# Kernel optimization log

Hardware: AMD Instinct MI355X
Metric: run time of the kernel (lower is better)

Reference implementation:

```python
import jax, jax.numpy as jnp
import numpy as np


def _cell(x, h, c, Wih, Whh, bih, bhh):
    # PyTorch LSTMCell: gates = x@Wih^T + bih + h@Whh^T + bhh, gate order i,f,g,o
    g = x @ Wih.T + bih + h @ Whh.T + bhh
    i, f, gg, o = jnp.split(g, 4, axis=-1)
    c_new = jax.nn.sigmoid(f) * c + jax.nn.sigmoid(i) * jnp.tanh(gg)
    h_new = jax.nn.sigmoid(o) * jnp.tanh(c_new)
    return h_new, c_new


def _forward(input, covariates, W_ih0, W_hh0, b_ih0, b_hh0,
             W_ih_r, W_hh_r, b_ih_r, b_hh_r, Wl, bl, future):
    B, T, _ = input.shape
    H = W_hh0.shape[1]
    Lm1 = W_ih_r.shape[0]  # number of stacked cells after layer 0

    # conditioning inputs: concat series with covariates -> [T, B, input_dim]
    xs = jnp.swapaxes(jnp.concatenate([input, covariates[:, :T, :]], axis=2), 0, 1)

    h0 = jnp.zeros((B, H), input.dtype)
    c0 = jnp.zeros((B, H), input.dtype)
    hr = jnp.zeros((Lm1, B, H), input.dtype)
    cr = jnp.zeros((Lm1, B, H), input.dtype)

    def run(state, x_t):
        h0, c0, hr, cr = state
        h0, c0 = _cell(x_t, h0, c0, W_ih0, W_hh0, b_ih0, b_hh0)
        prev = h0
        hs, cs = [], []
        for n in range(Lm1):  # static small loop over layers
            hn, cn = _cell(prev, hr[n], cr[n], W_ih_r[n], W_hh_r[n], b_ih_r[n], b_hh_r[n])
            hs.append(hn); cs.append(cn)
            prev = hn
        out = prev @ Wl.T + bl  # [B, output_dim]
        return (h0, c0, jnp.stack(hs), jnp.stack(cs)), out

    state, outs_cond = jax.lax.scan(run, (h0, c0, hr, cr), xs)  # outs_cond: [T,B,out]

    if future > 0:
        cov_f = jnp.swapaxes(covariates[:, T:T + future, :], 0, 1)  # [F,B,cov]

        def fut(carry, cov_t):
            state, out = carry
            x_t = jnp.concatenate([out, cov_t], axis=1)
            state, out = run(state, x_t)
            return (state, out), out

        _, outs_fut = jax.lax.scan(fut, (state, outs_cond[-1]), cov_f)
        outs = jnp.concatenate([outs_cond, outs_fut], axis=0)
    else:
        outs = outs_cond
    return jnp.swapaxes(outs, 0, 1)  # [B, T+future, output_dim]


def setup_inputs() -> dict:
    key = jax.random.key(0)
    ks = jax.random.split(key, 12)
    B, T, F = 512, 256, 64
    H, IN, COV, OUT, L = 1024, 8, 7, 1, 4
    s = 0.05
    return {
        "input": jax.random.normal(ks[0], (B, T, OUT), dtype=jnp.float32),
        "covariates": jax.random.normal(ks[1], (B, T + F, COV), dtype=jnp.float32),
        "W_ih0": jax.random.normal(ks[2], (4 * H, IN), dtype=jnp.float32) * s,
        "W_hh0": jax.random.normal(ks[3], (4 * H, H), dtype=jnp.float32) * s,
        "b_ih0": jax.random.normal(ks[4], (4 * H,), dtype=jnp.float32) * s,
        "b_hh0": jax.random.normal(ks[5], (4 * H,), dtype=jnp.float32) * s,
        "W_ih_r": jax.random.normal(ks[6], (L - 1, 4 * H, H), dtype=jnp.float32) * s,
        "W_hh_r": jax.random.normal(ks[7], (L - 1, 4 * H, H), dtype=jnp.float32) * s,
        "b_ih_r": jax.random.normal(ks[8], (L - 1, 4 * H), dtype=jnp.float32) * s,
        "b_hh_r": jax.random.normal(ks[9], (L - 1, 4 * H), dtype=jnp.float32) * s,
        "Wl": jax.random.normal(ks[10], (OUT, H), dtype=jnp.float32) * s,
        "bl": jax.random.normal(ks[11], (OUT,), dtype=jnp.float32) * s,
        "future": F,
    }


def reference(input, covariates, W_ih0, W_hh0, b_ih0, b_hh0,
              W_ih_r, W_hh_r, b_ih_r, b_hh_r, Wl, bl, future):
    return _forward(input, covariates, W_ih0, W_hh0, b_ih0, b_hh0,
                    W_ih_r, W_hh_r, b_ih_r, b_hh_r, Wl, bl, future)
```

## Files before the change

### kernel.cpp

```cpp
#include <hip/hip_runtime.h>

typedef _Float16 f16;
typedef __attribute__((ext_vector_type(8))) _Float16 half8;
typedef __attribute__((ext_vector_type(4))) float f32x4;
typedef __attribute__((ext_vector_type(4))) unsigned int uint4v;

#define B_   512
#define T_   256
#define TT_  320
#define KB0  33
#define KBR  64
#define NSLOT 12

#define AUX_COHERENT 17

struct PP {
  const f16* Wt[4];
  f16* xh[4][2];
  float* cst;
  const float* bias;
  const float* input;
  const float* cov;
  const float* Wl;
  const float* blp;
  float* out;
  unsigned* cnt;
};

__device__ __forceinline__ void gload16(const void* g, void* l) {
  __builtin_amdgcn_global_load_lds((const __attribute__((address_space(1))) void*)g,
                                   (__attribute__((address_space(3))) void*)l,
                                   16, 0, 0);
}
__device__ __forceinline__ void gload16c(const void* g, void* l) {
  __builtin_amdgcn_global_load_lds((const __attribute__((address_space(1))) void*)g,
                                   (__attribute__((address_space(3))) void*)l,
                                   16, 0, AUX_COHERENT);
}

__device__ __forceinline__ float sigf(float x) {
  return __builtin_amdgcn_rcpf(1.f + __builtin_amdgcn_exp2f(-1.44269504f * x));
}
__device__ __forceinline__ float tanhf_(float x) {
  return 2.f * __builtin_amdgcn_rcpf(1.f + __builtin_amdgcn_exp2f(-2.88539008f * x)) - 1.f;
}

__device__ __forceinline__ int haddr(int k, int m) {
  return (k >> 5) * 16384 + (m >> 4) * 512 + ((m & 15) + ((k & 31) >> 3) * 16) * 8 + (k & 7);
}

#define WAITBAR(vm) asm volatile("s_waitcnt vmcnt(" #vm ") lgkmcnt(0)\n\ts_barrier" ::: "memory")

__global__ __launch_bounds__(512, 2) void lstm_cond(PP P)
{
  __shared__ f16 lds[6][12288];
  const int tid = threadIdx.x;
  const int ln = tid & 63, w = tid >> 6;
  const int mg = w >> 2, ng = w & 3;
  const int cid = blockIdx.x >> 6, bb = blockIdx.x & 63;
  const int mb2 = bb >> 4, nb2 = bb & 15;
  const int m0 = mb2 * 128;
  const int l = cid;

  const f16* __restrict__ Wt = P.Wt[l];
  const int KB   = (l == 0) ? KB0 : KBR;
  const int koff = (l == 0) ? 32 : 1024;
  const float* __restrict__ bias4 = P.bias + l * 4096;
  float* __restrict__ cst = P.cst + (size_t)l * 524288;
  const int col = (nb2 * 4 + ng) * 16 + (ln & 15);
  const float bi  = bias4[col];
  const float bff = bias4[1024 + col];
  const float bgg = bias4[2048 + col];
  const float bo  = bias4[3072 + col];
  const float wl  = (l == 3) ? P.Wl[col] : 0.f;

  for (int s = 0; s <= 258; ++s) {
    if (s > 0) {
      if (tid == 0) {
        while (__hip_atomic_load(&P.cnt[s - 1], __ATOMIC_RELAXED,
                                 __HIP_MEMORY_SCOPE_AGENT) < 256u)
          __builtin_amdgcn_s_sleep(8);
      }
      __syncthreads();
    }

    const int t = s - l;
    if (t >= 0 && t < T_) {
      const int p = t & 1, q = p ^ 1;
      const f16* __restrict__ src = P.xh[l][p];
      f16* __restrict__ selfd     = P.xh[l][q];
      f16* __restrict__ nextd     = (l < 3) ? P.xh[l + 1][p] : nullptr;

      if (l == 0 && nb2 == 0 && tid < 128)
        __hip_atomic_store(&P.out[(size_t)(m0 + tid) * TT_ + t], P.blp[0],
                           __ATOMIC_RELAXED, __HIP_MEMORY_SCOPE_AGENT);

      auto stage_slab = [&](int slot, int kb) {
        if (l == 0 && kb == 0) {
          int mf = tid >> 6, r = ln & 15, kgrp = ln >> 4;
          int brow = m0 + mf * 16 + r;
          half8 v;
          #pragma unroll
          for (int j = 0; j < 8; ++j) v[j] = (f16)0.f;
          if (kgrp == 0) {
            v[0] = (f16)P.input[brow * T_ + t];
            const float* cp = P.cov + ((size_t)brow * TT_ + t) * 7;
            #pragma unroll
            for (int j = 1; j < 8; ++j) v[j] = (f16)cp[j - 1];
          }
          *(half8*)&lds[slot][tid * 8] = v;
        } else {
          gload16c(src + (size_t)kb * 16384 + mb2 * 4096 + tid * 8, &lds[slot][tid * 8]);
        }
        {
          const int e0 = tid, e1 = tid + 512;
          gload16(Wt + ((size_t)((nb2 * 4 + (e0 >> 8)) * KB + kb)) * 2048 + (e0 & 255) * 8,
                  &lds[slot][4096 + e0 * 8]);
          gload16(Wt + ((size_t)((nb2 * 4 + (e1 >> 8)) * KB + kb)) * 2048 + (e1 & 255) * 8,
                  &lds[slot][4096 + e1 * 8]);
        }
      };

      f32x4 acc[4][4];
      #pragma unroll
      for (int m = 0; m < 4; ++m)
        #pragma unroll
        for (int g = 0; g < 4; ++g) { acc[m][g][0]=0.f; acc[m][g][1]=0.f; acc[m][g][2]=0.f; acc[m][g][3]=0.f; }

      #pragma unroll
      for (int r = 0; r < 5; ++r) stage_slab(r, r);
      for (int i = 0; i < KB; ++i) {
        int ahead = KB - 1 - i; if (ahead > 4) ahead = 4;
        switch (ahead) {
          case 4:  WAITBAR(12); break;
          case 3:  WAITBAR(9);  break;
          case 2:  WAITBAR(6);  break;
          case 1:  WAITBAR(3);  break;
          default: WAITBAR(0);  break;
        }
        const int slot = i % 6;
        const half8* A  = (const half8*)&lds[slot][0];
        const half8* Bp = (const half8*)&lds[slot][4096];
        half8 a[4], b[4];
        #pragma unroll
        for (int m = 0; m < 4; ++m) a[m] = A[(mg * 4 + m) * 64 + ln];
        #pragma unroll
        for (int g = 0; g < 4; ++g) b[g] = Bp[ng * 256 + g * 64 + ln];
        if (i + 5 < KB) stage_slab((i + 5) % 6, i + 5);
        #pragma unroll
        for (int m = 0; m < 4; ++m)
          #pragma unroll
          for (int g = 0; g < 4; ++g)
            acc[m][g] = __builtin_amdgcn_mfma_f32_16x16x32_f16(a[m], b[g], acc[m][g], 0, 0, 0);
      }

      #pragma unroll
      for (int m = 0; m < 4; ++m) {
        const int rowb = m0 + (mg * 4 + m) * 16 + (ln >> 4) * 4;
        #pragma unroll
        for (int r = 0; r < 4; ++r) {
          const int row = rowb + r;
          float gi = acc[m][0][r] + bi;
          float gf = acc[m][1][r] + bff;
          float gg = acc[m][2][r] + bgg;
          float go = acc[m][3][r] + bo;
          float* cp = cst + (size_t)row * 1024 + col;
          float cn = sigf(gf) * (*cp) + sigf(gi) * tanhf_(gg);
          float h  = sigf(go) * tanhf_(cn);
          *cp = cn;
          f16 hh = (f16)h;
          unsigned short hbits = __builtin_bit_cast(unsigned short, hh);
          __hip_atomic_store((unsigned short*)&selfd[haddr(koff + col, row)], hbits,
                             __ATOMIC_RELAXED, __HIP_MEMORY_SCOPE_AGENT);
          if (l < 3) {
            __hip_atomic_store((unsigned short*)&nextd[haddr(col, row)], hbits,
                               __ATOMIC_RELAXED, __HIP_MEMORY_SCOPE_AGENT);
          } else {
            float val = h * wl;
            val += __shfl_xor(val, 1);
            val += __shfl_xor(val, 2);
            val += __shfl_xor(val, 4);
            val += __shfl_xor(val, 8);
            if ((ln & 15) == 0) atomicAdd(P.out + (size_t)row * TT_ + t, val);
          }
        }
      }
    }

    __syncthreads();
    if (tid == 0)
      __hip_atomic_fetch_add(&P.cnt[s], 1u, __ATOMIC_RELAXED, __HIP_MEMORY_SCOPE_AGENT);
  }
}

__global__ __launch_bounds__(512) void lstm_cells(PP P, int d, int lbeg, int lend, int tlim)
{
  __shared__ f16 lds[NSLOT][6144];
  const int tid = threadIdx.x;
  const int ln = tid & 63, w = tid >> 6;
  const int mg = w & 1, kg = w >> 1;
  const int nb = blockIdx.x & 63, mb = blockIdx.x >> 6;
  const int m0 = mb * 128, n0 = nb * 16;

  for (int l = lbeg; l <= lend; ++l) {
    const int t = d - l;
    if (t < 0 || t >= tlim) continue;

    const int p = t & 1, q = p ^ 1;
    const f16* __restrict__ Wt = P.Wt[l];
    const int KB   = (l == 0) ? KB0 : KBR;
    const int mode = (l == 0) ? 0 : ((l == 3) ? 2 : 1);
    const int koff = (l == 0) ? 32 : 1024;
    const f16* __restrict__ src   = P.xh[l][p];
    f16* __restrict__ selfd       = P.xh[l][q];
    f16* __restrict__ nextd       = (l < 3) ? P.xh[l + 1][p] : nullptr;
    const float* __restrict__ bias4 = P.bias + l * 4096;
    float* __restrict__ cst = P.cst + (size_t)l * 524288;

    if (mode == 0 && nb == 0 && tid < 128) P.out[(size_t)(m0 + tid) * TT_ + t] = P.blp[0];

    auto stage_slab = [&](int slot, int kb) {
      if (mode == 0 && kb == 0) {
        int mf = tid >> 6, r = ln & 15, kgrp = ln >> 4;
        int brow = m0 + mf * 16 + r;
        half8 v;
        #pragma unroll
        for (int j = 0; j < 8; ++j) v[j] = (f16)0.f;
        if (kgrp == 0) {
          float x0 = (t < T_) ? P.input[brow * T_ + t] : P.out[(size_t)brow * TT_ + (t - 1)];
          v[0] = (f16)x0;
          const float* cp = P.cov + ((size_t)brow * TT_ + t) * 7;
          #pragma unroll
          for (int j = 1; j < 8; ++j) v[j] = (f16)cp[j - 1];
        }
        *(half8*)&lds[slot][tid * 8] = v;
      } else {
        gload16(src + (size_t)kb * 16384 + mb * 4096 + tid * 8, &lds[slot][tid * 8]);
      }
      if (tid < 256)
        gload16(Wt + ((size_t)(nb * KB + kb)) * 2048 + tid * 8, &lds[slot][4096 + tid * 8]);
    };
    auto stage_round = [&](int r) {
      int base = (r % 3) * 4;
      #pragma unroll
      for (int j = 0; j < 4; ++j) {
        int kb = r * 4 + j;
        if (kb >= KB) kb = KB - 1;
        stage_slab(base + j, kb);
      }
    };

    f32x4 acc[4][4];
    #pragma unroll
    for (int m = 0; m < 4; ++m)
      #pragma unroll
      for (int g = 0; g < 4; ++g) { acc[m][g][0]=0.f; acc[m][g][1]=0.f; acc[m][g][2]=0.f; acc[m][g][3]=0.f; }

    const int R = (KB + 3) >> 2;
    stage_round(0); stage_round(1);
    for (int i = 0; i < R; ++i) {
      if (i < R - 1) { if (w < 4) WAITBAR(8); else WAITBAR(4); }
      else           { WAITBAR(0); }
      const int kb = i * 4 + kg;
      const int slot = (i % 3) * 4 + kg;
      const half8* A  = (const half8*)&lds[slot][0];
      const half8* Bp = (const half8*)&lds[slot][4096];
      const bool live = (kb < KB);
      half8 a0, a1, a2, a3, b0, b1, b2, b3;
      if (live) {
        a0 = A[(mg * 4 + 0) * 64 + ln];
        a1 = A[(mg * 4 + 1) * 64 + ln];
        a2 = A[(mg * 4 + 2) * 64 + ln];
        a3 = A[(mg * 4 + 3) * 64 + ln];
        b0 = Bp[ln]; b1 = Bp[64 + ln]; b2 = Bp[128 + ln]; b3 = Bp[192 + ln];
      }
      if (i + 2 < R) stage_round(i + 2);
      if (live) {
        acc[0][0] = __builtin_amdgcn_mfma_f32_16x16x32_f16(a0, b0, acc[0][0], 0, 0, 0);
        acc[0][1] = __builtin_amdgcn_mfma_f32_16x16x32_f16(a0, b1, acc[0][1], 0, 0, 0);
        acc[0][2] = __builtin_amdgcn_mfma_f32_16x16x32_f16(a0, b2, acc[0][2], 0, 0, 0);
        acc[0][3] = __builtin_amdgcn_mfma_f32_16x16x32_f16(a0, b3, acc[0][3], 0, 0, 0);
        acc[1][0] = __builtin_amdgcn_mfma_f32_16x16x32_f16(a1, b0, acc[1][0], 0, 0, 0);
        acc[1][1] = __builtin_amdgcn_mfma_f32_16x16x32_f16(a1, b1, acc[1][1], 0, 0, 0);
        acc[1][2] = __builtin_amdgcn_mfma_f32_16x16x32_f16(a1, b2, acc[1][2], 0, 0, 0);
        acc[1][3] = __builtin_amdgcn_mfma_f32_16x16x32_f16(a1, b3, acc[1][3], 0, 0, 0);
        acc[2][0] = __builtin_amdgcn_mfma_f32_16x16x32_f16(a2, b0, acc[2][0], 0, 0, 0);
        acc[2][1] = __builtin_amdgcn_mfma_f32_16x16x32_f16(a2, b1, acc[2][1], 0, 0, 0);
        acc[2][2] = __builtin_amdgcn_mfma_f32_16x16x32_f16(a2, b2, acc[2][2], 0, 0, 0);
        acc[2][3] = __builtin_amdgcn_mfma_f32_16x16x32_f16(a2, b3, acc[2][3], 0, 0, 0);
        acc[3][0] = __builtin_amdgcn_mfma_f32_16x16x32_f16(a3, b0, acc[3][0], 0, 0, 0);
        acc[3][1] = __builtin_amdgcn_mfma_f32_16x16x32_f16(a3, b1, acc[3][1], 0, 0, 0);
        acc[3][2] = __builtin_amdgcn_mfma_f32_16x16x32_f16(a3, b2, acc[3][2], 0, 0, 0);
        acc[3][3] = __builtin_amdgcn_mfma_f32_16x16x32_f16(a3, b3, acc[3][3], 0, 0, 0);
      }
    }

    __syncthreads();
    float* red = (float*)&lds[0][0];
    #pragma unroll
    for (int m = 0; m < 4; ++m)
      #pragma unroll
      for (int g = 0; g < 4; ++g)
        *(f32x4*)&red[w * 4096 + (m * 4 + g) * 256 + ln * 4] = acc[m][g];
    __syncthreads();
    f32x4 facc[4];
    #pragma unroll
    for (int g = 0; g < 4; ++g) { facc[g][0]=0.f; facc[g][1]=0.f; facc[g][2]=0.f; facc[g][3]=0.f; }
    const int mgw = w >> 2, mlw = w & 3;
    #pragma unroll
    for (int kg2 = 0; kg2 < 4; ++kg2) {
      const int wsrc = kg2 * 2 + mgw;
      #pragma unroll
      for (int g = 0; g < 4; ++g) {
        f32x4 pv = *(const f32x4*)&red[wsrc * 4096 + (mlw * 4 + g) * 256 + ln * 4];
        facc[g][0] += pv[0]; facc[g][1] += pv[1]; facc[g][2] += pv[2]; facc[g][3] += pv[3];
      }
    }
    __syncthreads();

    const int col = n0 + (ln & 15);
    const int rowb = m0 + w * 16 + (ln >> 4) * 4;
    const float bi  = bias4[col];
    const float bff = bias4[1024 + col];
    const float bgg = bias4[2048 + col];
    const float bo  = bias4[3072 + col];
    const float wl  = (mode == 2) ? P.Wl[col] : 0.f;
    #pragma unroll
    for (int r = 0; r < 4; ++r) {
      const int row = rowb + r;
      float gi = facc[0][r] + bi;
      float gf = facc[1][r] + bff;
      float gg = facc[2][r] + bgg;
      float go = facc[3][r] + bo;
      float* cp = cst + (size_t)row * 1024 + col;
      float cn = sigf(gf) * (*cp) + sigf(gi) * tanhf_(gg);
      float h  = sigf(go) * tanhf_(cn);
      *cp = cn;
      f16 hh = (f16)h;
      selfd[haddr(koff + col, row)] = hh;
      if (mode != 2) {
        nextd[haddr(col, row)] = hh;
      } else {
        float val = h * wl;
        val += __shfl_xor(val, 1);
        val += __shfl_xor(val, 2);
        val += __shfl_xor(val, 4);
        val += __shfl_xor(val, 8);
        if ((ln & 15) == 0) atomicAdd(P.out + (size_t)row * TT_ + t, val);
      }
    }
  }
}

__global__ void zero_ws(uint4v* pz, int n)
{
  int i = blockIdx.x * 256 + threadIdx.x;
  if (i < n) { uint4v z; z[0] = 0u; z[1] = 0u; z[2] = 0u; z[3] = 0u; pz[i] = z; }
}

__global__ void pack_weights(const float* __restrict__ Wih0, const float* __restrict__ Whh0,
                             const float* __restrict__ Wihr, const float* __restrict__ Whhr,
                             f16* __restrict__ Wt0, f16* __restrict__ Wt1,
                             f16* __restrict__ Wt2, f16* __restrict__ Wt3)
{
  const int layer = blockIdx.y;
  const size_t e = (size_t)blockIdx.x * 256 + threadIdx.x;
  const int KB = layer ? KBR : KB0;
  if (e >= (size_t)64 * KB * 2048) return;
  const int panel = (int)(e >> 11), win = (int)(e & 2047);
  const int g = win >> 9, lane = (win >> 3) & 63, j = win & 7;
  const int nb = panel / KB, kb = panel - nb * KB;
  const int n = nb * 16 + (lane & 15);
  const int k = kb * 32 + (lane >> 4) * 8 + j;
  const int jr = g * 1024 + n;
  float v;
  if (layer == 0) {
    if (k < 8)       v = Wih0[jr * 8 + k];
    else if (k < 32) v = 0.f;
    else             v = Whh0[(size_t)jr * 1024 + (k - 32)];
  } else {
    const size_t base = (size_t)(layer - 1) * 4096 * 1024 + (size_t)jr * 1024;
    v = (k < 1024) ? Wihr[base + k] : Whhr[base + (k - 1024)];
  }
  f16 hv = (f16)v;
  if      (layer == 0) Wt0[e] = hv;
  else if (layer == 1) Wt1[e] = hv;
  else if (layer == 2) Wt2[e] = hv;
  else                 Wt3[e] = hv;
}

__global__ void pack_bias(const float* __restrict__ bih0, const float* __restrict__ bhh0,
                          const float* __restrict__ bihr, const float* __restrict__ bhhr,
                          float* __restrict__ bias)
{
  const int idx = blockIdx.x * 256 + threadIdx.x;
  const int lyr = idx >> 12, j = idx & 4095;
  bias[idx] = (lyr == 0) ? (bih0[j] + bhh0[j])
                         : (bihr[(lyr - 1) * 4096 + j] + bhhr[(lyr - 1) * 4096 + j]);
}

extern "C" void kernel_launch(void* const* d_in, const int* in_sizes, int n_in,
                              void* d_out, int out_size, void* d_ws, size_t ws_size,
                              hipStream_t stream)
{
  const float* input = (const float*)d_in[0];
  const float* cov   = (const float*)d_in[1];
  const float* Wih0  = (const float*)d_in[2];
  const float* Whh0  = (const float*)d_in[3];
  const float* bih0  = (const float*)d_in[4];
  const float* bhh0  = (const float*)d_in[5];
  const float* Wihr  = (const float*)d_in[6];
  const float* Whhr  = (const float*)d_in[7];
  const float* bihr  = (const float*)d_in[8];
  const float* bhhr  = (const float*)d_in[9];
  const float* Wl    = (const float*)d_in[10];
  const float* blp   = (const float*)d_in[11];
  float* out = (float*)d_out;
  char* ws = (char*)d_ws;

  const size_t XH0 = 1081344, XHR = 2097152;
  PP Pv;
  Pv.xh[0][0] = (f16*)(ws);            Pv.xh[0][1] = (f16*)(ws + XH0);
  Pv.xh[1][0] = (f16*)(ws + 2162688);  Pv.xh[1][1] = (f16*)(ws + 2162688 + XHR);
  Pv.xh[2][0] = (f16*)(ws + 6356992);  Pv.xh[2][1] = (f16*)(ws + 6356992 + XHR);
  Pv.xh[3][0] = (f16*)(ws + 10551296); Pv.xh[3][1] = (f16*)(ws + 10551296 + XHR);
  Pv.cst     = (float*)(ws + 14745600);
  Pv.cnt     = (unsigned*)(ws);
  float* bias = (float*)(ws + 23134208);
  f16* Wt0 = (f16*)(ws + 23199744);
  f16* Wt1 = (f16*)(ws + 31850496);
  f16* Wt2 = (f16*)(ws + 48627712);
  f16* Wt3 = (f16*)(ws + 65404928);
  Pv.Wt[0] = Wt0; Pv.Wt[1] = Wt1; Pv.Wt[2] = Wt2; Pv.Wt[3] = Wt3;
  Pv.bias = bias; Pv.input = input; Pv.cov = cov;
  Pv.Wl = Wl; Pv.blp = blp; Pv.out = out;

  pack_weights<<<dim3(32768, 4), 256, 0, stream>>>(Wih0, Whh0, Wihr, Whhr, Wt0, Wt1, Wt2, Wt3);
  pack_bias<<<64, 256, 0, stream>>>(bih0, bhh0, bihr, bhhr, bias);
  zero_ws<<<5648, 256, 0, stream>>>((uint4v*)ws, 23134208 / 16);

  void* args[] = { &Pv };
  hipLaunchCooperativeKernel(reinterpret_cast<void*>(&lstm_cond),
                             dim3(256), dim3(512), args, 0, stream);

  for (int t = T_; t < TT_; ++t)
    for (int l = 0; l < 4; ++l)
      lstm_cells<<<256, 512, 0, stream>>>(Pv, t + l, l, l, TT_);
}
```

Baseline: 18.17 ms.

## Decouple A and B staging in lstm_cond with deeper activation prefetch

Splits the shared-memory ring into separate activation (12-slot) and weight (3-slot) buffers. Activations are now prefetched 10 slabs ahead and weights 2 ahead. The first two weight slabs of the next timestep are issued before the inter-block spin wait, so weight loads overlap the cross-block synchronisation. MFMA issue priority is raised with s_setprio. Launch bounds drop to one block per CU to fit the larger LDS footprint, which costs occupancy, and redundant clamped loads are issued at the end of the K loop.

After: 19.39 ms. +6.7%, slower.

```diff
diff --git a/kernel.cpp b/kernel.cpp
--- a/kernel.cpp
+++ b/kernel.cpp
@@ -51,9 +51,10 @@
 
 #define WAITBAR(vm) asm volatile("s_waitcnt vmcnt(" #vm ") lgkmcnt(0)\n\ts_barrier" ::: "memory")
 
-__global__ __launch_bounds__(512, 2) void lstm_cond(PP P)
-{
-  __shared__ f16 lds[6][12288];
+__global__ __launch_bounds__(512, 1) void lstm_cond(PP P)
+{
+  __shared__ f16 lds_a[12][4096];
+  __shared__ f16 lds_b[3][8192];
   const int tid = threadIdx.x;
   const int ln = tid & 63, w = tid >> 6;
   const int mg = w >> 2, ng = w & 3;
@@ -74,7 +75,19 @@
   const float bo  = bias4[3072 + col];
   const float wl  = (l == 3) ? P.Wl[col] : 0.f;
 
+  auto stageB = [&](int slot, int kb) {
+    const int e0 = tid, e1 = tid + 512;
+    gload16(Wt + ((size_t)((nb2 * 4 + (e0 >> 8)) * KB + kb)) * 2048 + (e0 & 255) * 8,
+            &lds_b[slot][e0 * 8]);
+    gload16(Wt + ((size_t)((nb2 * 4 + (e1 >> 8)) * KB + kb)) * 2048 + (e1 & 255) * 8,
+            &lds_b[slot][e1 * 8]);
+  };
+
+  if (l == 0) { stageB(0, 0); stageB(1, 1); }
+
   for (int s = 0; s <= 258; ++s) {
+    const int t = s - l;
+
     if (s > 0) {
       if (tid == 0) {
         while (__hip_atomic_load(&P.cnt[s - 1], __ATOMIC_RELAXED,
@@ -84,7 +97,6 @@
       __syncthreads();
     }
 
-    const int t = s - l;
     if (t >= 0 && t < T_) {
       const int p = t & 1, q = p ^ 1;
       const f16* __restrict__ src = P.xh[l][p];
@@ -95,29 +107,22 @@
         __hip_atomic_store(&P.out[(size_t)(m0 + tid) * TT_ + t], P.blp[0],
                            __ATOMIC_RELAXED, __HIP_MEMORY_SCOPE_AGENT);
 
-      auto stage_slab = [&](int slot, int kb) {
+      auto stageA = [&](int slot, int kb) {
         if (l == 0 && kb == 0) {
           int mf = tid >> 6, r = ln & 15, kgrp = ln >> 4;
           int brow = m0 + mf * 16 + r;
           half8 v;
           #pragma unroll
-          for (int j = 0; j < 8; ++j) v[j] = (f16)0.f;
+          for (int z = 0; z < 8; ++z) v[z] = (f16)0.f;
           if (kgrp == 0) {
             v[0] = (f16)P.input[brow * T_ + t];
             const float* cp = P.cov + ((size_t)brow * TT_ + t) * 7;
             #pragma unroll
-            for (int j = 1; j < 8; ++j) v[j] = (f16)cp[j - 1];
+            for (int z = 1; z < 8; ++z) v[z] = (f16)cp[z - 1];
           }
-          *(half8*)&lds[slot][tid * 8] = v;
+          *(half8*)&lds_a[slot][tid * 8] = v;
         } else {
-          gload16c(src + (size_t)kb * 16384 + mb2 * 4096 + tid * 8, &lds[slot][tid * 8]);
-        }
-        {
-          const int e0 = tid, e1 = tid + 512;
-          gload16(Wt + ((size_t)((nb2 * 4 + (e0 >> 8)) * KB + kb)) * 2048 + (e0 & 255) * 8,
-                  &lds[slot][4096 + e0 * 8]);
-          gload16(Wt + ((size_t)((nb2 * 4 + (e1 >> 8)) * KB + kb)) * 2048 + (e1 & 255) * 8,
-                  &lds[slot][4096 + e1 * 8]);
+          gload16c(src + (size_t)kb * 16384 + mb2 * 4096 + tid * 8, &lds_a[slot][tid * 8]);
         }
       };
 
@@ -128,31 +133,32 @@
         for (int g = 0; g < 4; ++g) { acc[m][g][0]=0.f; acc[m][g][1]=0.f; acc[m][g][2]=0.f; acc[m][g][3]=0.f; }
 
       #pragma unroll
-      for (int r = 0; r < 5; ++r) stage_slab(r, r);
+      for (int kb = 0; kb < 10; ++kb) stageA(kb, kb);
+
       for (int i = 0; i < KB; ++i) {
-        int ahead = KB - 1 - i; if (ahead > 4) ahead = 4;
-        switch (ahead) {
-          case 4:  WAITBAR(12); break;
-          case 3:  WAITBAR(9);  break;
-          case 2:  WAITBAR(6);  break;
-          case 1:  WAITBAR(3);  break;
-          default: WAITBAR(0);  break;
-        }
-        const int slot = i % 6;
-        const half8* A  = (const half8*)&lds[slot][0];
-        const half8* Bp = (const half8*)&lds[slot][4096];
+        if (i == 0)      { if (l == 0) { WAITBAR(11); } else { WAITBAR(9); } }
+        else if (i == 1) { WAITBAR(11); }
+        else             { WAITBAR(3); }
+        const half8* A  = (const half8*)&lds_a[i % 12][0];
+        const half8* Bp = (const half8*)&lds_b[i % 3][0];
         half8 a[4], b[4];
         #pragma unroll
         for (int m = 0; m < 4; ++m) a[m] = A[(mg * 4 + m) * 64 + ln];
         #pragma unroll
         for (int g = 0; g < 4; ++g) b[g] = Bp[ng * 256 + g * 64 + ln];
-        if (i + 5 < KB) stage_slab((i + 5) % 6, i + 5);
+        int ka = i + 10; if (ka >= KB) ka = KB - 1;
+        stageA((i + 10) % 12, ka);
+        int kbb = i + 2; if (kbb >= KB) kbb = KB - 1;
+        stageB((i + 2) % 3, kbb);
+        __builtin_amdgcn_s_setprio(1);
         #pragma unroll
         for (int m = 0; m < 4; ++m)
           #pragma unroll
           for (int g = 0; g < 4; ++g)
             acc[m][g] = __builtin_amdgcn_mfma_f32_16x16x32_f16(a[m], b[g], acc[m][g], 0, 0, 0);
-      }
+        __builtin_amdgcn_s_setprio(0);
+      }
+      WAITBAR(0);
 
       #pragma unroll
       for (int m = 0; m < 4; ++m) {
@@ -190,6 +196,8 @@
     __syncthreads();
     if (tid == 0)
       __hip_atomic_fetch_add(&P.cnt[s], 1u, __ATOMIC_RELAXED, __HIP_MEMORY_SCOPE_AGENT);
+    const int tn = (s + 1) - l;
+    if (tn >= 0 && tn < T_) { stageB(0, 0); stageB(1, 1); }
   }
 }
 
```
